# Performance work log

Measured on AMD Instinct MI355X. Metric: run time of the kernel, lower is better.

Reference implementation:

```python
import jax, jax.numpy as jnp
import numpy as np

N, E, D, H = 15000, 300000, 128, 4
Dh = D // H
EPS = 1e-5

def gelu(x):
    return jax.nn.gelu(x, approximate=False)

def lin(x, W, b=None):
    y = x @ W.T
    return y + b if b is not None else y

def bnorm(x, g, b):
    # BatchNorm1d (training stats, biased var) over the row dim
    m = x.mean(0)
    v = x.var(0)
    return (x - m) * jax.lax.rsqrt(v + EPS) * g + b

def setup_inputs() -> dict:
    key = jax.random.key(0)
    ks = iter(jax.random.split(key, 64))
    def W(o, i):
        return jax.random.normal(next(ks), (o, i), jnp.float32) / jnp.sqrt(i)
    z = lambda o: jnp.zeros((o,), jnp.float32)
    o1 = lambda o: jnp.ones((o,), jnp.float32)
    inp = {
        'h_V': jax.random.normal(next(ks), (N, D), jnp.float32),
        'h_E': jax.random.normal(next(ks), (E, D), jnp.float32),
        'edge_idx': jax.random.randint(next(ks), (2, E), 0, N, jnp.int64),
        'batch_id': jnp.sort(jax.random.randint(next(ks), (N,), 0, 30, jnp.int32)),
        # NeighborAttention.W_V MLP: num_in(256)->128->128->128
        'Wv1': W(D, 2 * D), 'bv1': z(D), 'Wv2': W(D, D), 'bv2': z(D), 'Wv3': W(D, D), 'bv3': z(D),
        # NeighborAttention.Bias MLP: 3*128->128->128->num_heads
        'Wb1': W(D, 3 * D), 'bb1': z(D), 'Wb2': W(D, D), 'bb2': z(D), 'Wb3': W(H, D), 'bb3': z(H),
        # W_O (no bias)
        'Wo': W(D, D),
        # norms 0/1 on nodes
        'g0': o1(D), 'b0': z(D), 'g1': o1(D), 'b1': z(D),
        # dense FFN 128->512->128
        'Wd1': W(4 * D, D), 'bd1': z(4 * D), 'Wd2': W(D, 4 * D), 'bd2': z(D),
        # EdgeMLP: 384->128->128->128 plus edge norm
        'We1': W(D, 3 * D), 'be1': z(D), 'We2': W(D, D), 'be2': z(D), 'We3': W(D, D), 'be3': z(D),
        'ge': o1(D), 'bEn': z(D),
    }
    return inp

def reference(h_V, h_E, edge_idx, batch_id,
              Wv1, bv1, Wv2, bv2, Wv3, bv3,
              Wb1, bb1, Wb2, bb2, Wb3, bb3,
              Wo, g0, b0, g1, b1,
              Wd1, bd1, Wd2, bd2,
              We1, be1, We2, be2, We3, be3, ge, bEn):
    src, dst = edge_idx[0], edge_idx[1]
    # --- NeighborAttention (sparse) ---
    h_EV = jnp.concatenate([h_E, h_V[dst]], axis=-1)              # (E, 2D)
    bias_in = jnp.concatenate([h_V[src], h_EV], axis=-1)          # (E, 3D)
    w = lin(gelu(lin(gelu(lin(bias_in, Wb1, bb1)), Wb2, bb2)), Wb3, bb3)
    w = w * (1.0 / jnp.sqrt(jnp.float32(Dh)))                     # (E, H)
    V = lin(gelu(lin(gelu(lin(h_EV, Wv1, bv1)), Wv2, bv2)), Wv3, bv3).reshape(E, H, Dh)
    # scatter_softmax over edges grouped by src (center_id)
    m = jax.ops.segment_max(w, src, num_segments=N)               # (N, H)
    e = jnp.exp(w - m[src])
    s = jax.ops.segment_sum(e, src, num_segments=N)
    attend = e / s[src]                                           # (E, H)
    agg = jax.ops.segment_sum(attend[..., None] * V, src, num_segments=N).reshape(N, D)
    dh = agg @ Wo.T
    # --- residual + norm + FFN ---
    h_V = bnorm(h_V + dh, g0, b0)
    dh = lin(gelu(lin(h_V, Wd1, bd1)), Wd2, bd2)
    h_V = bnorm(h_V + dh, g1, b1)
    # --- EdgeMLP update ---
    h_EV2 = jnp.concatenate([h_V[src], h_E, h_V[dst]], axis=-1)   # (E, 3D)
    msg = lin(gelu(lin(gelu(lin(h_EV2, We1, be1)), We2, be2)), We3, be3)
    h_E = bnorm(h_E + msg, ge, bEn)
    # Context with node_context=edge_context=0 is a no-op
    return h_V, h_E
```

## Files before the change

kernel.cpp:

```cpp
#include <hip/hip_runtime.h>
#include <hip/hip_bf16.h>
#include <math.h>


#define NN 15000
#define EE 300000

typedef short s16x8 __attribute__((ext_vector_type(8)));
typedef float f32x4 __attribute__((ext_vector_type(4)));
#define MFMA16(a,b,c) __builtin_amdgcn_mfma_f32_16x16x32_bf16((a),(b),(c),0,0,0)

#define O_Wot  0
#define O_Wd1t (O_Wot  + 128*128)
#define O_Wd2t (O_Wd1t + 128*512)
#define O_BF   (O_Wd2t + 512*128)
#define O_WB   (O_BF + 107520)
#define O_M    (O_WB + EE*4)
#define O_S    (O_M + NN*4)
#define O_AGG  (O_S + NN*4)
#define O_STAT (O_AGG + NN*128)
#define O_AB   (O_STAT + 768)
#define O_XB   (O_AB + 768)
#define O_HID  (O_XB + NN*128)

#define UB_Wb1 0
#define UB_Wb2 49152
#define UB_Wb3 65536
#define UB_Wv1 67584
#define UB_Wv2 100352
#define UB_Wv3 116736
#define UB_We1 133120
#define UB_We2 182272
#define UB_We3 198656

__device__ inline float gelu_f(float x){
  return 0.5f*x*(1.0f + erff(x*0.70710678118654752f));
}
__device__ inline unsigned fenc(float f){
  unsigned u = __float_as_uint(f);
  return (u & 0x80000000u) ? ~u : (u | 0x80000000u);
}
__device__ inline float fdec(unsigned u){
  return __uint_as_float((u & 0x80000000u) ? (u & 0x7fffffffu) : ~u);
}
__device__ inline ushort bfb(float f){
  __bf16 h = (__bf16)f;
  return __builtin_bit_cast(unsigned short, h);
}


struct EMem {
  ushort act[128][128];
  int   idx[256];
  float cp[256];
};

union FB { s16x8 v; ushort u[8]; };

__device__ inline s16x8 load_x8(const float* __restrict__ p){
  float4 a = *(const float4*)p;
  float4 b = *(const float4*)(p+4);
  FB r;
  r.u[0]=bfb(a.x); r.u[1]=bfb(a.y); r.u[2]=bfb(a.z); r.u[3]=bfb(a.w);
  r.u[4]=bfb(b.x); r.u[5]=bfb(b.y); r.u[6]=bfb(b.z); r.u[7]=bfb(b.w);
  return r.v;
}

__device__ inline void st_act4(ushort (*act)[128], int e, int obase,
                               float g0,float g1,float g2,float g3){
  short4 s;
  s.x=(short)bfb(g0); s.y=(short)bfb(g1); s.z=(short)bfb(g2); s.w=(short)bfb(g3);
  *(short4*)&act[e][obase ^ ((e&7)<<3)] = s;
}
__device__ inline s16x8 ld_act(ushort (*act)[128], int e, int k0){
  return *(const s16x8*)&act[e][k0 ^ ((e&7)<<3)];
}

__device__ inline void zacc(f32x4 (&a)[4][4]){
  #pragma unroll
  for(int i=0;i<4;++i)
    #pragma unroll
    for(int j=0;j<4;++j) a[i][j] = (f32x4){0.f,0.f,0.f,0.f};
}

__device__ inline void mm_lds(const ushort* __restrict__ Wb, ushort (*act)[128],
                              int wm, int wn, int el, int kq, f32x4 (&acc)[4][4])
{
  #pragma unroll
  for (int kt=0; kt<4; ++kt){
    s16x8 af[4], bfr[4];
    #pragma unroll
    for (int mt=0;mt<4;++mt)
      af[mt] = *(const s16x8*)&Wb[(wm*64+mt*16+el)*128 + kt*32 + kq*8];
    #pragma unroll
    for (int nt=0;nt<4;++nt)
      bfr[nt] = ld_act(act, wn*64+nt*16+el, kt*32+kq*8);
    #pragma unroll
    for (int mt=0;mt<4;++mt)
      #pragma unroll
      for (int nt=0;nt<4;++nt)
        acc[mt][nt] = MFMA16(af[mt], bfr[nt], acc[mt][nt]);
  }
}

__device__ inline void intf(f32x4 (&acc)[4][4], const float* __restrict__ bias,
                            ushort (*act)[128], int wm, int wn, int el, int kq)
{
  #pragma unroll
  for (int mt=0;mt<4;++mt){
    int obase = wm*64+mt*16+kq*4;
    float4 bb = *(const float4*)&bias[obase];
    #pragma unroll
    for (int nt=0;nt<4;++nt){
      int e = wn*64+nt*16+el;
      st_act4(act, e, obase,
        gelu_f(acc[mt][nt][0]+bb.x), gelu_f(acc[mt][nt][1]+bb.y),
        gelu_f(acc[mt][nt][2]+bb.z), gelu_f(acc[mt][nt][3]+bb.w));
    }
  }
}

__device__ inline void edge_l1_3seg(const float* __restrict__ gV, const float* __restrict__ gI,
    const int* idx, const ushort* __restrict__ W1, int rowbase,
    int wm, int wn, int el, int kq, f32x4 (&acc)[4][4])
{
  #pragma unroll
  for (int seg=0; seg<3; ++seg){
    const float* rp[4];
    #pragma unroll
    for (int nt=0; nt<4; ++nt){
      int eloc = wn*64+nt*16+el;
      int g;
      if (seg==0) g = idx[eloc];
      else if (seg==1){ int e=rowbase+eloc; g = (e<EE)?e:(EE-1); }
      else g = idx[128+eloc];
      rp[nt] = ((seg==1)?gI:gV) + (size_t)g*128 + kq*8;
    }
    #pragma unroll
    for (int kt=0; kt<4; ++kt){
      s16x8 af[4], bfr[4];
      #pragma unroll
      for (int mt=0;mt<4;++mt)
        af[mt] = *(const s16x8*)&W1[(wm*64+mt*16+el)*384 + seg*128 + kt*32 + kq*8];
      #pragma unroll
      for (int nt=0;nt<4;++nt)
        bfr[nt] = load_x8(rp[nt] + kt*32);
      #pragma unroll
      for (int mt=0;mt<4;++mt)
        #pragma unroll
        for (int nt=0;nt<4;++nt)
          acc[mt][nt] = MFMA16(af[mt], bfr[nt], acc[mt][nt]);
    }
  }
}

__global__ void kA_mfma(const float* __restrict__ hV, const float* __restrict__ hE,
    const int* __restrict__ eidx,
    const ushort* __restrict__ W1, const ushort* __restrict__ W2, const ushort* __restrict__ W3,
    const float* __restrict__ b1, const float* __restrict__ b2, const float* __restrict__ b3,
    float* __restrict__ wbuf, unsigned* __restrict__ mArr)
{
  __shared__ EMem sm;
  int t = threadIdx.x, lane = t&63, wave = t>>6;
  int el = lane&15, kq = lane>>4, wm = wave>>1, wn = wave&1;
  int rowbase = blockIdx.x*128;
  if (t<128){ int e=rowbase+t; if(e>=EE) e=EE-1; sm.idx[t]=eidx[e]; sm.idx[128+t]=eidx[EE+e]; }
  __syncthreads();
  f32x4 acc[4][4]; zacc(acc);
  edge_l1_3seg(hV, hE, sm.idx, W1, rowbase, wm, wn, el, kq, acc);
  intf(acc, b1, sm.act, wm, wn, el, kq);
  __syncthreads();
  zacc(acc);
  mm_lds(W2, sm.act, wm, wn, el, kq, acc);
  __syncthreads();
  intf(acc, b2, sm.act, wm, wn, el, kq);
  __syncthreads();
  f32x4 a3[2]; a3[0]=(f32x4){0.f,0.f,0.f,0.f}; a3[1]=(f32x4){0.f,0.f,0.f,0.f};
  #pragma unroll
  for (int kt=0;kt<4;++kt){
    s16x8 af = *(const s16x8*)&W3[el*128 + kt*32 + kq*8];
    #pragma unroll
    for (int q=0;q<2;++q){
      s16x8 bv = ld_act(sm.act, wave*32+q*16+el, kt*32+kq*8);
      a3[q] = MFMA16(af, bv, a3[q]);
    }
  }
  if (kq==0){
    #pragma unroll
    for (int q=0;q<2;++q){
      int eloc = wave*32+q*16+el, e = rowbase+eloc;
      if (e<EE){
        const float SC = 0.17677669529663687f;
        float4 w;
        w.x=(a3[q][0]+b3[0])*SC; w.y=(a3[q][1]+b3[1])*SC;
        w.z=(a3[q][2]+b3[2])*SC; w.w=(a3[q][3]+b3[3])*SC;
        *(float4*)&wbuf[e*4] = w;
        unsigned s4 = (unsigned)sm.idx[eloc]*4;
        atomicMax(&mArr[s4+0],fenc(w.x));
        atomicMax(&mArr[s4+1],fenc(w.y));
        atomicMax(&mArr[s4+2],fenc(w.z));
        atomicMax(&mArr[s4+3],fenc(w.w));
      }
    }
  }
}

__global__ void kB(const int* __restrict__ eidx, const unsigned* __restrict__ mArr,
                   float* __restrict__ wbuf, float* __restrict__ sArr)
{
  int tid = blockIdx.x*256 + threadIdx.x;
  if (tid >= EE*4) return;
  int e = tid >> 2, h = tid & 3;
  int srcn = eidx[e];
  float ex = expf(wbuf[tid] - fdec(mArr[srcn*4 + h]));
  wbuf[tid] = ex;
  atomicAdd(&sArr[srcn*4 + h], ex);
}

__global__ void kC_mfma(const float* __restrict__ hV, const float* __restrict__ hE,
    const int* __restrict__ eidx,
    const ushort* __restrict__ W1, const ushort* __restrict__ W2, const ushort* __restrict__ W3,
    const float* __restrict__ b1, const float* __restrict__ b2, const float* __restrict__ b3,
    const float* __restrict__ wbuf, const float* __restrict__ sArr,
    float* __restrict__ agg)
{
  __shared__ EMem sm;
  int t = threadIdx.x, lane = t&63, wave = t>>6;
  int el = lane&15, kq = lane>>4, wm = wave>>1, wn = wave&1;
  int rowbase = blockIdx.x*128;
  if (t<128){ int e=rowbase+t; if(e>=EE) e=EE-1; sm.idx[t]=eidx[e]; sm.idx[128+t]=eidx[EE+e]; }
  __syncthreads();
  f32x4 acc[4][4]; zacc(acc);
  #pragma unroll
  for (int seg=0; seg<2; ++seg){
    const float* rp[4];
    #pragma unroll
    for (int nt=0; nt<4; ++nt){
      int eloc = wn*64+nt*16+el;
      int g;
      if (seg==0){ int e=rowbase+eloc; g = (e<EE)?e:(EE-1); }
      else g = sm.idx[128+eloc];
      rp[nt] = ((seg==0)?hE:hV) + (size_t)g*128 + kq*8;
    }
    #pragma unroll
    for (int kt=0; kt<4; ++kt){
      s16x8 af[4], bfr[4];
      #pragma unroll
      for (int mt=0;mt<4;++mt)
        af[mt] = *(const s16x8*)&W1[(wm*64+mt*16+el)*256 + seg*128 + kt*32 + kq*8];
      #pragma unroll
      for (int nt=0;nt<4;++nt)
        bfr[nt] = load_x8(rp[nt] + kt*32);
      #pragma unroll
      for (int mt=0;mt<4;++mt)
        #pragma unroll
        for (int nt=0;nt<4;++nt)
          acc[mt][nt] = MFMA16(af[mt], bfr[nt], acc[mt][nt]);
    }
  }
  intf(acc, b1, sm.act, wm, wn, el, kq);
  __syncthreads();
  zacc(acc);
  mm_lds(W2, sm.act, wm, wn, el, kq, acc);
  __syncthreads();
  intf(acc, b2, sm.act, wm, wn, el, kq);
  __syncthreads();
  zacc(acc);
  mm_lds(W3, sm.act, wm, wn, el, kq, acc);
  #pragma unroll
  for (int nt=0;nt<4;++nt){
    int eloc = wn*64+nt*16+el, e = rowbase+eloc;
    if (e < EE){
      int sn = sm.idx[eloc];
      float4 wv = *(const float4*)&wbuf[e*4];
      float4 sv = *(const float4*)&sArr[sn*4];
      float at4[4] = {wv.x/sv.x, wv.y/sv.y, wv.z/sv.z, wv.w/sv.w};
      #pragma unroll
      for (int mt=0;mt<4;++mt){
        int o = wm*64+mt*16+kq*4;
        float4 bb = *(const float4*)&b3[o];
        float a = at4[o>>5];
        float* ap = &agg[(size_t)sn*128 + o];
        atomicAdd(ap+0, a*(acc[mt][nt][0]+bb.x));
        atomicAdd(ap+1, a*(acc[mt][nt][1]+bb.y));
        atomicAdd(ap+2, a*(acc[mt][nt][2]+bb.z));
        atomicAdd(ap+3, a*(acc[mt][nt][3]+bb.w));
      }
    }
  }
}

__global__ void kI_mfma(const float* __restrict__ hVfin, const float* __restrict__ hE,
    const int* __restrict__ eidx,
    const ushort* __restrict__ W1, const ushort* __restrict__ W2, const ushort* __restrict__ W3,
    const float* __restrict__ b1, const float* __restrict__ b2, const float* __restrict__ b3,
    float* __restrict__ hEout, float* __restrict__ stat)
{
  __shared__ EMem sm;
  int t = threadIdx.x, lane = t&63, wave = t>>6;
  int el = lane&15, kq = lane>>4, wm = wave>>1, wn = wave&1;
  int rowbase = blockIdx.x*128;
  if (t<128){ int e=rowbase+t; if(e>=EE) e=EE-1; sm.idx[t]=eidx[e]; sm.idx[128+t]=eidx[EE+e]; }
  __syncthreads();
  f32x4 acc[4][4]; zacc(acc);
  edge_l1_3seg(hVfin, hE, sm.idx, W1, rowbase, wm, wn, el, kq, acc);
  intf(acc, b1, sm.act, wm, wn, el, kq);
  __syncthreads();
  zacc(acc);
  mm_lds(W2, sm.act, wm, wn, el, kq, acc);
  __syncthreads();
  intf(acc, b2, sm.act, wm, wn, el, kq);
  __syncthreads();
  zacc(acc);
  mm_lds(W3, sm.act, wm, wn, el, kq, acc);
  float ps[4][4], pq[4][4];
  #pragma unroll
  for (int mt=0;mt<4;++mt)
    #pragma unroll
    for (int r=0;r<4;++r){ ps[mt][r]=0.f; pq[mt][r]=0.f; }
  #pragma unroll
  for (int nt=0;nt<4;++nt){
    int eloc = wn*64+nt*16+el, e = rowbase+eloc;
    if (e < EE){
      #pragma unroll
      for (int mt=0;mt<4;++mt){
        int o = wm*64+mt*16+kq*4;
        float4 bb = *(const float4*)&b3[o];
        float4 h0 = *(const float4*)&hE[(size_t)e*128+o];
        float4 v;
        v.x = h0.x+acc[mt][nt][0]+bb.x;
        v.y = h0.y+acc[mt][nt][1]+bb.y;
        v.z = h0.z+acc[mt][nt][2]+bb.z;
        v.w = h0.w+acc[mt][nt][3]+bb.w;
        *(float4*)&hEout[(size_t)e*128+o] = v;
        ps[mt][0]+=v.x; ps[mt][1]+=v.y; ps[mt][2]+=v.z; ps[mt][3]+=v.w;
        pq[mt][0]+=v.x*v.x; pq[mt][1]+=v.y*v.y; pq[mt][2]+=v.z*v.z; pq[mt][3]+=v.w*v.w;
      }
    }
  }
  __syncthreads();
  sm.cp[t] = 0.f;
  __syncthreads();
  #pragma unroll
  for (int mt=0;mt<4;++mt){
    int o = wm*64+mt*16+kq*4;
    #pragma unroll
    for (int r=0;r<4;++r){
      atomicAdd(&sm.cp[o+r], ps[mt][r]);
      atomicAdd(&sm.cp[128+o+r], pq[mt][r]);
    }
  }
  __syncthreads();
  atomicAdd(&stat[t], sm.cp[t]);
}

struct SMem {
  float act[128][132];
  float ws[16][128];
  int   idx[256];
  float cp[256];
};

__device__ inline void zero8(float (&a)[8][8]){
  #pragma unroll
  for (int i=0;i<8;++i)
    #pragma unroll
    for (int j=0;j<8;++j) a[i][j]=0.f;
}

__device__ inline void stage_chunk(const float* __restrict__ src, int width, int kbase,
                                   const int* idxArr, int rowbase, int limit,
                                   float (*act)[132], int t)
{
  __syncthreads();
  int k = t & 127, half = t >> 7;
  const float* sp = src + kbase + k;
  #pragma unroll
  for (int i = 0; i < 64; i += 4){
    int r = half*64 + i;
    float v[4];
    #pragma unroll
    for (int j = 0; j < 4; ++j){
      int rr = r + j;
      int g = idxArr ? idxArr[rr] : ((rowbase + rr < limit) ? (rowbase + rr) : (limit-1));
      v[j] = sp[g*width];
    }
    *(float4*)&act[k][r] = make_float4(v[0],v[1],v[2],v[3]);
  }
  __syncthreads();
}

__device__ inline void stage_aff(const float* __restrict__ src, const float* __restrict__ ab,
                                 int rowbase, int limit, float (*act)[132], int t)
{
  __syncthreads();
  int k = t & 127, half = t >> 7;
  float a = ab[k], c = ab[128+k];
  const float* sp = src + k;
  #pragma unroll
  for (int i = 0; i < 64; i += 4){
    int r = half*64 + i;
    float v[4];
    #pragma unroll
    for (int j = 0; j < 4; ++j){
      int rr = r + j;
      int g = (rowbase + rr < limit) ? (rowbase + rr) : (limit-1);
      v[j] = fmaf(sp[g*128], a, c);
    }
    *(float4*)&act[k][r] = make_float4(v[0],v[1],v[2],v[3]);
  }
  __syncthreads();
}

__device__ inline void gemm128(const float* __restrict__ Wt, int ldw, int kbase, int ccol,
                               float (&acc)[8][8], float (*act)[132], float (*ws)[128], int t)
{
  int c0 = (t & 15)*8, r0 = (t >> 4)*8;
  for (int ks = 0; ks < 128; ks += 16){
    __syncthreads();
    {
      int kk = t >> 4, c = (t & 15)*8;
      const float* wp = Wt + (kbase + ks + kk)*ldw + ccol + c;
      float4 w0 = *(const float4*)wp;
      float4 w1 = *(const float4*)(wp + 4);
      *(float4*)&ws[kk][c]   = w0;
      *(float4*)&ws[kk][c+4] = w1;
    }
    __syncthreads();
    #pragma unroll
    for (int kk = 0; kk < 16; ++kk){
      int k = ks + kk;
      float4 xa = *(float4*)&act[k][r0];
      float4 xb = *(float4*)&act[k][r0+4];
      float4 wa = *(float4*)&ws[kk][c0];
      float4 wb = *(float4*)&ws[kk][c0+4];
      float x[8] = {xa.x,xa.y,xa.z,xa.w,xb.x,xb.y,xb.z,xb.w};
      float w[8] = {wa.x,wa.y,wa.z,wa.w,wb.x,wb.y,wb.z,wb.w};
      #pragma unroll
      for (int ri=0;ri<8;++ri)
        #pragma unroll
        for (int ci=0;ci<8;++ci)
          acc[ri][ci] = fmaf(x[ri], w[ci], acc[ri][ci]);
    }
  }
}

__device__ inline void block_stats(const float (&ps)[8], const float (&pq)[8],
                                   float* __restrict__ stat, float* cp, int t)
{
  int c0=(t&15)*8;
  __syncthreads();
  cp[t] = 0.f;
  __syncthreads();
  #pragma unroll
  for (int ci=0;ci<8;++ci){
    atomicAdd(&cp[c0+ci], ps[ci]);
    atomicAdd(&cp[128+c0+ci], pq[ci]);
  }
  __syncthreads();
  if (t < 128){
    atomicAdd(&stat[t], cp[t]);
    atomicAdd(&stat[128+t], cp[128+t]);
  }
}

struct TP { const float* s[3]; float* d[3]; };

__global__ void kT(TP a){
  const int Os[3]={128,512,128};
  const int Is[3]={128,128,512};
  int b = blockIdx.x, mi = 0, off = 0;
  for (;;){
    int nb = (Os[mi]*Is[mi] + 4095) >> 12;
    if (b < off + nb) break;
    off += nb; ++mi;
  }
  int O = Os[mi], I = Is[mi], sz = O*I;
  int e0 = (b - off) * 4096;
  int eEnd = (e0 + 4096 < sz) ? (e0 + 4096) : sz;
  for (int e = e0 + (int)threadIdx.x; e < eEnd; e += 256){
    int o = e / I, i = e - o*I;
    a.d[mi][i*O + o] = a.s[mi][e];
  }
}

struct CP9 { const float* s[9]; };

__global__ void kConv(CP9 a, ushort* __restrict__ dst){
  const int SZ[9]   = {49152,16384,2048,32768,16384,16384,49152,16384,16384};
  const int SRCSZ[9]= {49152,16384, 512,32768,16384,16384,49152,16384,16384};
  int b = blockIdx.x, mi=0, off=0;
  for(;;){ int nb=(SZ[mi]+1023)>>10; if (b<off+nb) break; off+=nb; ++mi; }
  int base=0;
  for(int j=0;j<mi;++j) base+=SZ[j];
  int e0=(b-off)*1024;
  int eE=(e0+1024<SZ[mi])?(e0+1024):SZ[mi];
  for (int i=e0+(int)threadIdx.x; i<eE; i+=256){
    float v = (i < SRCSZ[mi]) ? a.s[mi][i] : 0.f;
    dst[base+i] = bfb(v);
  }
}

__global__ __launch_bounds__(256,2) void kD(
    const float* __restrict__ hV, const float* __restrict__ aggM, const float* __restrict__ Wot,
    float* __restrict__ xbuf, float* __restrict__ stat)
{
  __shared__ SMem sm;
  int t = threadIdx.x;
  int rowbase = blockIdx.x * 128;
  float acc[8][8];
  zero8(acc);
  stage_chunk(aggM, 128, 0, nullptr, rowbase, NN, sm.act, t);
  gemm128(Wot, 128, 0, 0, acc, sm.act, sm.ws, t);
  int c0=(t&15)*8, r0=(t>>4)*8;
  float ps[8]={0,0,0,0,0,0,0,0}, pq[8]={0,0,0,0,0,0,0,0};
  #pragma unroll
  for (int ri=0;ri<8;++ri){
    int g = rowbase + r0 + ri;
    if (g < NN){
      float4 h0 = *(const float4*)&hV[g*128+c0];
      float4 h1 = *(const float4*)&hV[g*128+c0+4];
      float hv[8]={h0.x,h0.y,h0.z,h0.w,h1.x,h1.y,h1.z,h1.w};
      float v[8];
      #pragma unroll
      for (int ci=0;ci<8;++ci){
        v[ci]=hv[ci]+acc[ri][ci];
        ps[ci]+=v[ci]; pq[ci]+=v[ci]*v[ci];
      }
      *(float4*)&xbuf[g*128+c0]   = make_float4(v[0],v[1],v[2],v[3]);
      *(float4*)&xbuf[g*128+c0+4] = make_float4(v[4],v[5],v[6],v[7]);
    }
  }
  block_stats(ps,pq,stat,sm.cp,t);
}

__global__ void kFin(const float* __restrict__ stat, const float* __restrict__ gw,
                     const float* __restrict__ bw, float* __restrict__ ab, float invcnt)
{
  int t = threadIdx.x;
  float mean = stat[t]*invcnt;
  float var  = fmaxf(stat[128+t]*invcnt - mean*mean, 0.f);
  float inv  = rsqrtf(var + 1e-5f);
  float a = inv * gw[t];
  ab[t] = a;
  ab[128+t] = fmaf(-mean, a, bw[t]);
}

__global__ __launch_bounds__(256,2) void kF1(
    const float* __restrict__ xbuf, const float* __restrict__ ab0,
    const float* __restrict__ Wd1t, const float* __restrict__ bd1,
    float* __restrict__ hidden)
{
  __shared__ SMem sm;
  int t = threadIdx.x;
  int rowbase = blockIdx.x * 128;
  stage_aff(xbuf, ab0, rowbase, NN, sm.act, t);
  int c0=(t&15)*8, r0=(t>>4)*8;
  for (int cc=0; cc<4; ++cc){
    float acc[8][8];
    zero8(acc);
    gemm128(Wd1t, 512, 0, cc*128, acc, sm.act, sm.ws, t);
    float bd[8];
    #pragma unroll
    for (int ci=0;ci<8;++ci) bd[ci]=bd1[cc*128+c0+ci];
    #pragma unroll
    for (int ri=0;ri<8;++ri){
      int g = rowbase + r0 + ri;
      if (g < NN){
        float v[8];
        #pragma unroll
        for (int ci=0;ci<8;++ci) v[ci]=gelu_f(acc[ri][ci]+bd[ci]);
        *(float4*)&hidden[g*512+cc*128+c0]   = make_float4(v[0],v[1],v[2],v[3]);
        *(float4*)&hidden[g*512+cc*128+c0+4] = make_float4(v[4],v[5],v[6],v[7]);
      }
    }
  }
}

__global__ __launch_bounds__(256,2) void kF2(
    const float* __restrict__ xbuf, const float* __restrict__ hidden,
    const float* __restrict__ ab0, const float* __restrict__ Wd2t, const float* __restrict__ bd2,
    float* __restrict__ hVout, float* __restrict__ stat)
{
  __shared__ SMem sm;
  int t = threadIdx.x;
  int rowbase = blockIdx.x * 128;
  float acc[8][8];
  zero8(acc);
  for (int cc=0; cc<4; ++cc){
    stage_chunk(hidden, 512, cc*128, nullptr, rowbase, NN, sm.act, t);
    gemm128(Wd2t, 128, cc*128, 0, acc, sm.act, sm.ws, t);
  }
  int c0=(t&15)*8, r0=(t>>4)*8;
  float a0v[8],c0v[8],bd[8];
  #pragma unroll
  for (int ci=0;ci<8;++ci){ a0v[ci]=ab0[c0+ci]; c0v[ci]=ab0[128+c0+ci]; bd[ci]=bd2[c0+ci]; }
  float ps[8]={0,0,0,0,0,0,0,0}, pq[8]={0,0,0,0,0,0,0,0};
  #pragma unroll
  for (int ri=0;ri<8;++ri){
    int g = rowbase + r0 + ri;
    if (g < NN){
      float4 x0 = *(const float4*)&xbuf[g*128+c0];
      float4 x1 = *(const float4*)&xbuf[g*128+c0+4];
      float xv[8]={x0.x,x0.y,x0.z,x0.w,x1.x,x1.y,x1.z,x1.w};
      float v[8];
      #pragma unroll
      for (int ci=0;ci<8;++ci){
        v[ci] = fmaf(xv[ci], a0v[ci], c0v[ci]) + acc[ri][ci] + bd[ci];
        ps[ci]+=v[ci]; pq[ci]+=v[ci]*v[ci];
      }
      *(float4*)&hVout[g*128+c0]   = make_float4(v[0],v[1],v[2],v[3]);
      *(float4*)&hVout[g*128+c0+4] = make_float4(v[4],v[5],v[6],v[7]);
    }
  }
  block_stats(ps,pq,stat,sm.cp,t);
}

__global__ void kNorm(float* __restrict__ x, const float* __restrict__ ab, int total)
{
  int i = (blockIdx.x*256 + (int)threadIdx.x)*4;
  if (i >= total) return;
  float4 v = *(float4*)&x[i];
  int c = i & 127;
  v.x = fmaf(v.x, ab[c],   ab[128+c]);
  v.y = fmaf(v.y, ab[c+1], ab[128+c+1]);
  v.z = fmaf(v.z, ab[c+2], ab[128+c+2]);
  v.w = fmaf(v.w, ab[c+3], ab[128+c+3]);
  *(float4*)&x[i] = v;
}

extern "C" void kernel_launch(void* const* d_in, const int* in_sizes, int n_in,
                              void* d_out, int out_size, void* d_ws, size_t ws_size,
                              hipStream_t stream)
{
  const float* hV  =(const float*)d_in[0];
  const float* hE  =(const float*)d_in[1];
  const int*   eidx=(const int*)  d_in[2];
  const float* Wv1 =(const float*)d_in[4];
  const float* bv1 =(const float*)d_in[5];
  const float* Wv2 =(const float*)d_in[6];
  const float* bv2 =(const float*)d_in[7];
  const float* Wv3 =(const float*)d_in[8];
  const float* bv3 =(const float*)d_in[9];
  const float* Wb1 =(const float*)d_in[10];
  const float* bb1 =(const float*)d_in[11];
  const float* Wb2 =(const float*)d_in[12];
  const float* bb2 =(const float*)d_in[13];
  const float* Wb3 =(const float*)d_in[14];
  const float* bb3 =(const float*)d_in[15];
  const float* Wo  =(const float*)d_in[16];
  const float* g0  =(const float*)d_in[17];
  const float* b0  =(const float*)d_in[18];
  const float* g1  =(const float*)d_in[19];
  const float* b1  =(const float*)d_in[20];
  const float* Wd1 =(const float*)d_in[21];
  const float* bd1 =(const float*)d_in[22];
  const float* Wd2 =(const float*)d_in[23];
  const float* bd2 =(const float*)d_in[24];
  const float* We1 =(const float*)d_in[25];
  const float* be1 =(const float*)d_in[26];
  const float* We2 =(const float*)d_in[27];
  const float* be2 =(const float*)d_in[28];
  const float* We3 =(const float*)d_in[29];
  const float* be3 =(const float*)d_in[30];
  const float* ge  =(const float*)d_in[31];
  const float* bEn =(const float*)d_in[32];

  float* W  = (float*)d_ws;
  float* dO = (float*)d_out;
  ushort* WB = (ushort*)(W + O_BF);

  TP tp;
  tp.s[0]=Wo;  tp.d[0]=W+O_Wot;
  tp.s[1]=Wd1; tp.d[1]=W+O_Wd1t;
  tp.s[2]=Wd2; tp.d[2]=W+O_Wd2t;
  kT<<<36,256,0,stream>>>(tp);

  CP9 c9;
  c9.s[0]=Wb1; c9.s[1]=Wb2; c9.s[2]=Wb3;
  c9.s[3]=Wv1; c9.s[4]=Wv2; c9.s[5]=Wv3;
  c9.s[6]=We1; c9.s[7]=We2; c9.s[8]=We3;
  kConv<<<210,256,0,stream>>>(c9, WB);

  hipMemsetAsync(W + O_M, 0, (size_t)(O_AB - O_M)*sizeof(float), stream);

  kA_mfma<<<(EE+127)/128,256,0,stream>>>(hV,hE,eidx, WB+UB_Wb1,WB+UB_Wb2,WB+UB_Wb3,
                                         bb1,bb2,bb3, W+O_WB,(unsigned*)(W+O_M));
  kB<<<(EE*4+255)/256,256,0,stream>>>(eidx,(const unsigned*)(W+O_M), W+O_WB, W+O_S);
  kC_mfma<<<(EE+127)/128,256,0,stream>>>(hV,hE,eidx, WB+UB_Wv1,WB+UB_Wv2,WB+UB_Wv3,
                                         bv1,bv2,bv3, W+O_WB, W+O_S, W+O_AGG);

  kD<<<(NN+127)/128,256,0,stream>>>(hV, W+O_AGG, W+O_Wot, W+O_XB, W+O_STAT);
  kFin<<<1,128,0,stream>>>(W+O_STAT, g0, b0, W+O_AB, 1.0f/NN);
  kF1<<<(NN+127)/128,256,0,stream>>>(W+O_XB, W+O_AB, W+O_Wd1t, bd1, W+O_HID);
  kF2<<<(NN+127)/128,256,0,stream>>>(W+O_XB, W+O_HID, W+O_AB, W+O_Wd2t, bd2,
                                     dO, W+O_STAT+256);
  kFin<<<1,128,0,stream>>>(W+O_STAT+256, g1, b1, W+O_AB+256, 1.0f/NN);
  kNorm<<<(NN*128/4+255)/256,256,0,stream>>>(dO, W+O_AB+256, NN*128);

  kI_mfma<<<(EE+127)/128,256,0,stream>>>(dO, hE, eidx, WB+UB_We1,WB+UB_We2,WB+UB_We3,
                                         be1,be2,be3, dO+(size_t)NN*128, W+O_STAT+512);
  kFin<<<1,128,0,stream>>>(W+O_STAT+512, ge, bEn, W+O_AB+512, 1.0f/EE);
  kNorm<<<(EE*128/4+255)/256,256,0,stream>>>(dO+(size_t)NN*128, W+O_AB+512, EE*128);
}
```

Before: 1.923 ms.

## Sort edges by source via counting sort and segment-reduce attention aggregation in LDS

After: 1.642 ms. 14.6% less time.

```diff
diff --git a/kernel.cpp b/kernel.cpp
--- a/kernel.cpp
+++ b/kernel.cpp
@@ -22,6 +22,9 @@
 #define O_AB   (O_STAT + 768)
 #define O_XB   (O_AB + 768)
 #define O_HID  (O_XB + NN*128)
+#define O_PERM (O_HID + NN*512)
+#define O_CNT  (O_PERM + EE)
+#define O_CUR  (O_CNT + 15360)
 
 #define UB_Wb1 0
 #define UB_Wb2 49152
@@ -55,6 +58,12 @@
   float cp[256];
 };
 
+struct EMemC {
+  union { ushort act[128][128]; float vbuf[128][128]; };
+  int pe[128];
+  int idx[256];
+};
+
 union FB { s16x8 v; ushort u[8]; };
 
 __device__ inline s16x8 load_x8(const float* __restrict__ p){
@@ -151,6 +160,35 @@
         for (int nt=0;nt<4;++nt)
           acc[mt][nt] = MFMA16(af[mt], bfr[nt], acc[mt][nt]);
     }
+  }
+}
+
+__global__ void kHist(const int* __restrict__ eidx, int* __restrict__ cnt){
+  int e = blockIdx.x*256 + threadIdx.x;
+  if (e < EE) atomicAdd(&cnt[eidx[e]], 1);
+}
+
+__global__ void kScan(const int* __restrict__ cnt, int* __restrict__ cur){
+  __shared__ int part[256];
+  __shared__ int excl[256];
+  int t = threadIdx.x;
+  int base = t*60;
+  int s = 0;
+  for (int i=0;i<60;++i) s += cnt[base+i];
+  part[t] = s;
+  __syncthreads();
+  if (t==0){ int r=0; for (int i=0;i<256;++i){ excl[i]=r; r+=part[i]; } }
+  __syncthreads();
+  int run = excl[t];
+  for (int i=0;i<60;++i){ int c = cnt[base+i]; cur[base+i] = run; run += c; }
+}
+
+__global__ void kScat(const int* __restrict__ eidx, int* __restrict__ cur,
+                      int* __restrict__ perm){
+  int e = blockIdx.x*256 + threadIdx.x;
+  if (e < EE){
+    int p = atomicAdd(&cur[eidx[e]], 1);
+    perm[p] = e;
   }
 }
 
@@ -218,17 +256,23 @@
 }
 
 __global__ void kC_mfma(const float* __restrict__ hV, const float* __restrict__ hE,
-    const int* __restrict__ eidx,
+    const int* __restrict__ eidx, const int* __restrict__ perm,
     const ushort* __restrict__ W1, const ushort* __restrict__ W2, const ushort* __restrict__ W3,
     const float* __restrict__ b1, const float* __restrict__ b2, const float* __restrict__ b3,
     const float* __restrict__ wbuf, const float* __restrict__ sArr,
     float* __restrict__ agg)
 {
-  __shared__ EMem sm;
+  __shared__ EMemC sm;
   int t = threadIdx.x, lane = t&63, wave = t>>6;
   int el = lane&15, kq = lane>>4, wm = wave>>1, wn = wave&1;
   int rowbase = blockIdx.x*128;
-  if (t<128){ int e=rowbase+t; if(e>=EE) e=EE-1; sm.idx[t]=eidx[e]; sm.idx[128+t]=eidx[EE+e]; }
+  if (t<128){
+    int slot = rowbase + t; if (slot >= EE) slot = EE-1;
+    int pe = perm[slot];
+    sm.pe[t] = pe;
+    sm.idx[t] = eidx[pe];
+    sm.idx[128+t] = eidx[EE+pe];
+  }
   __syncthreads();
   f32x4 acc[4][4]; zacc(acc);
   #pragma unroll
@@ -237,9 +281,7 @@
     #pragma unroll
     for (int nt=0; nt<4; ++nt){
       int eloc = wn*64+nt*16+el;
-      int g;
-      if (seg==0){ int e=rowbase+eloc; g = (e<EE)?e:(EE-1); }
-      else g = sm.idx[128+eloc];
+      int g = (seg==0) ? sm.pe[eloc] : sm.idx[128+eloc];
       rp[nt] = ((seg==0)?hE:hV) + (size_t)g*128 + kq*8;
     }
     #pragma unroll
@@ -267,26 +309,49 @@
   __syncthreads();
   zacc(acc);
   mm_lds(W3, sm.act, wm, wn, el, kq, acc);
+  __syncthreads();
   #pragma unroll
   for (int nt=0;nt<4;++nt){
-    int eloc = wn*64+nt*16+el, e = rowbase+eloc;
-    if (e < EE){
-      int sn = sm.idx[eloc];
-      float4 wv = *(const float4*)&wbuf[e*4];
+    int e = wn*64+nt*16+el;
+    int slot = rowbase + e;
+    float at4[4];
+    if (slot < EE){
+      int pe = sm.pe[e];
+      int sn = sm.idx[e];
+      float4 wv = *(const float4*)&wbuf[pe*4];
       float4 sv = *(const float4*)&sArr[sn*4];
-      float at4[4] = {wv.x/sv.x, wv.y/sv.y, wv.z/sv.z, wv.w/sv.w};
-      #pragma unroll
-      for (int mt=0;mt<4;++mt){
-        int o = wm*64+mt*16+kq*4;
-        float4 bb = *(const float4*)&b3[o];
-        float a = at4[o>>5];
-        float* ap = &agg[(size_t)sn*128 + o];
-        atomicAdd(ap+0, a*(acc[mt][nt][0]+bb.x));
-        atomicAdd(ap+1, a*(acc[mt][nt][1]+bb.y));
-        atomicAdd(ap+2, a*(acc[mt][nt][2]+bb.z));
-        atomicAdd(ap+3, a*(acc[mt][nt][3]+bb.w));
+      at4[0]=wv.x/sv.x; at4[1]=wv.y/sv.y; at4[2]=wv.z/sv.z; at4[3]=wv.w/sv.w;
+    } else {
+      at4[0]=at4[1]=at4[2]=at4[3]=0.f;
+    }
+    #pragma unroll
+    for (int mt=0;mt<4;++mt){
+      int o = wm*64+mt*16+kq*4;
+      float4 bb = *(const float4*)&b3[o];
+      float a = at4[o>>5];
+      float4 v;
+      v.x = a*(acc[mt][nt][0]+bb.x);
+      v.y = a*(acc[mt][nt][1]+bb.y);
+      v.z = a*(acc[mt][nt][2]+bb.z);
+      v.w = a*(acc[mt][nt][3]+bb.w);
+      *(float4*)&sm.vbuf[e][o ^ ((e&7)<<2)] = v;
+    }
+  }
+  __syncthreads();
+  {
+    int col = t & 127, h2 = t >> 7;
+    int e0 = h2*64;
+    float run = 0.f;
+    int cursrc = sm.idx[e0];
+    for (int e = e0; e < e0+64; ++e){
+      int s = sm.idx[e];
+      if (s != cursrc){
+        atomicAdd(&agg[(size_t)cursrc*128 + col], run);
+        run = 0.f; cursrc = s;
       }
-    }
+      run += sm.vbuf[e][col ^ ((e&7)<<2)];
+    }
+    atomicAdd(&agg[(size_t)cursrc*128 + col], run);
   }
 }
 
@@ -682,12 +747,18 @@
   c9.s[6]=We1; c9.s[7]=We2; c9.s[8]=We3;
   kConv<<<210,256,0,stream>>>(c9, WB);
 
+  hipMemsetAsync(W + O_CNT, 0, 15360*sizeof(int), stream);
+  kHist<<<(EE+255)/256,256,0,stream>>>(eidx, (int*)(W+O_CNT));
+  kScan<<<1,256,0,stream>>>((const int*)(W+O_CNT), (int*)(W+O_CUR));
+  kScat<<<(EE+255)/256,256,0,stream>>>(eidx, (int*)(W+O_CUR), (int*)(W+O_PERM));
+
   hipMemsetAsync(W + O_M, 0, (size_t)(O_AB - O_M)*sizeof(float), stream);
 
   kA_mfma<<<(EE+127)/128,256,0,stream>>>(hV,hE,eidx, WB+UB_Wb1,WB+UB_Wb2,WB+UB_Wb3,
                                          bb1,bb2,bb3, W+O_WB,(unsigned*)(W+O_M));
   kB<<<(EE*4+255)/256,256,0,stream>>>(eidx,(const unsigned*)(W+O_M), W+O_WB, W+O_S);
-  kC_mfma<<<(EE+127)/128,256,0,stream>>>(hV,hE,eidx, WB+UB_Wv1,WB+UB_Wv2,WB+UB_Wv3,
+  kC_mfma<<<(EE+127)/128,256,0,stream>>>(hV,hE,eidx,(const int*)(W+O_PERM),
+                                         WB+UB_Wv1,WB+UB_Wv2,WB+UB_Wv3,
                                          bv1,bv2,bv3, W+O_WB, W+O_S, W+O_AGG);
 
   kD<<<(NN+127)/128,256,0,stream>>>(hV, W+O_AGG, W+O_Wot, W+O_XB, W+O_STAT);
```
